# Performance work log

Measured on AMD Instinct MI355X. Metric: run time of the kernel, lower is better.

Reference implementation:

```python
import jax, jax.numpy as jnp
import numpy as np

CONTEXT = 3  # config['context']
B, H, W = 8, 256, 256
NBR = 2 * CONTEXT  # number of similarity branches


def _conv(x, w, b):
    # x: [N, Cin, H, W], w: [Cout, Cin, kh, kw], SAME padding, stride 1
    y = jax.lax.conv_general_dilated(x, w, (1, 1), 'SAME',
                                     dimension_numbers=('NCHW', 'OIHW', 'NCHW'))
    return y + b[None, :, None, None]


def setup_inputs() -> dict:
    key = jax.random.key(0)
    ks = jax.random.split(key, 5)
    x = jax.random.normal(ks[0], (B, 2 * CONTEXT + 1, H, W), dtype=jnp.float32)
    # kaiming-ish scaled inits
    W1 = jax.random.normal(ks[1], (NBR, 64, 2, 3, 3), dtype=jnp.float32) * (2.0 / (64 * 9)) ** 0.5
    b1 = jnp.zeros((NBR, 64), dtype=jnp.float32)
    W2 = jax.random.normal(ks[2], (NBR, 1, 64, 1, 1), dtype=jnp.float32) * (2.0 / 1) ** 0.5 * 0.1
    b2 = jnp.zeros((NBR, 1), dtype=jnp.float32)
    Wm = jax.random.normal(ks[3], (7, 7, 3, 3), dtype=jnp.float32) * (2.0 / (7 * 9)) ** 0.5
    bm = jnp.zeros((7,), dtype=jnp.float32)
    return {'x': x, 'W1': W1, 'b1': b1, 'W2': W2, 'b2': b2, 'Wm': Wm, 'bm': bm}


def reference(x, W1, b1, W2, b2, Wm, bm):
    # mode == 'context' path just returns x; this implements the main path.
    base = x[:, CONTEXT:CONTEXT + 1]                                  # [B,1,H,W]
    checks = jnp.concatenate([x[:, :CONTEXT], x[:, CONTEXT + 1:]], axis=1)  # [B,6,H,W]
    check_e = checks[:, :, None]                                      # [B,6,1,H,W]
    base_e = jnp.broadcast_to(base[:, None], check_e.shape)           # [B,6,1,H,W]
    # channel order: pre-frames -> (base, check); post-frames -> (check, base)
    ch0 = jnp.concatenate([base_e[:, :CONTEXT], check_e[:, CONTEXT:]], axis=2 - 2 + 2)  # placeholder
    ch0 = jnp.concatenate([base_e[:, :CONTEXT], check_e[:, CONTEXT:]], axis=1)
    ch1 = jnp.concatenate([check_e[:, :CONTEXT], base_e[:, CONTEXT:]], axis=1)
    pairs = jnp.concatenate([ch0, ch1], axis=2)                       # [B,6,2,H,W]
    pairs = jnp.swapaxes(pairs, 0, 1)                                 # [6,B,2,H,W]

    def branch(pair, w1, bb1, w2, bb2):
        h = jax.nn.relu(_conv(pair, w1, bb1))                         # [B,64,H,W]
        return jax.nn.sigmoid(_conv(h, w2, bb2))                      # [B,1,H,W]

    sims = jax.vmap(branch)(pairs, W1, b1, W2, b2)                    # [6,B,1,H,W]
    weighted = sims[:, :, 0] * jnp.swapaxes(checks, 0, 1)             # [6,B,H,W]
    weighted = jnp.swapaxes(weighted, 0, 1)                           # [B,6,H,W]
    combined = jnp.concatenate([weighted[:, :CONTEXT], base, weighted[:, CONTEXT:]], axis=1)  # [B,7,H,W]
    return _conv(combined, Wm, bm)                                    # [B,7,H,W]
```

## Files before the change

kernel.cpp:

```cpp
#include <hip/hip_runtime.h>
#include <math.h>

#define Bn 8
#define Hn 256
#define Wn 256
#define HW (Hn * Wn)
#define ROWS 8
#define RP 264
#define ZW (20 * RP)

typedef __attribute__((ext_vector_type(8))) short bf16x8;
typedef __attribute__((ext_vector_type(4))) float f32x4;

__device__ __forceinline__ unsigned int pk_bits(unsigned int lo,
                                                unsigned int hi) {
  return __builtin_amdgcn_perm(hi, lo, 0x07060302u);
}
__device__ __forceinline__ unsigned int pk_bf16(float lo, float hi) {
  return pk_bits(__float_as_uint(lo), __float_as_uint(hi));
}

__device__ __constant__ const int T0c[8] = {0, 1, 2, 9, 10, 11, 3, 4};
__device__ __constant__ const int T1c[8] = {6, 7, 8, 15, 16, 17, 12, 13};
__device__ __constant__ const int T2c[8] = {5, 14, -1, -1, -1, -1, -1, -1};

__global__ __launch_bounds__(256) void sim_kernel(
    const float* __restrict__ x,
    const float* __restrict__ W1,
    const float* __restrict__ b1,
    const float* __restrict__ W2,
    const float* __restrict__ b2,
    float* __restrict__ comb)
{
  __shared__ float rowsF[20 * RP + 64];
  __shared__ uint4 wq[4][64];

  int bi = blockIdx.x;
  int n  = bi >> 8;
  int b  = (bi >> 5) & 7;
  int h0 = (bi & 31) * ROWS;
  int cc = (n < 3) ? n : n + 1;
  int t = threadIdx.x;

  const float* xb     = x + (size_t)b * 7 * HW;
  const float* basep  = xb + 3 * HW;
  const float* checkp = xb + (size_t)cc * HW;

  {
    int f = t >> 6, qq = (t >> 4) & 3, m = t & 15;
    int bsrc = (n < 3) ? 0 : 1;
    const float* wch = W1 + ((size_t)(n * 64 + 16 * f + m)) * 18;
    unsigned int kv[4];
#pragma unroll
    for (int jj = 0; jj < 4; ++jj) {
      int ja = 2 * jj, jb = 2 * jj + 1;
      int ta = (qq == 0) ? T0c[ja] : (qq == 1) ? T1c[ja]
               : (qq == 2) ? T2c[ja] : -1;
      int tb = (qq == 0) ? T0c[jb] : (qq == 1) ? T1c[jb]
               : (qq == 2) ? T2c[jb] : -1;
      float va = 0.f, vb = 0.f;
      if (ta >= 0) {
        int pl = ta / 9, rem = ta - pl * 9;
        va = wch[(pl ? 1 - bsrc : bsrc) * 9 + rem];
      }
      if (tb >= 0) {
        int pl = tb / 9, rem = tb - pl * 9;
        vb = wch[(pl ? 1 - bsrc : bsrc) * 9 + rem];
      }
      kv[jj] = pk_bf16(va, vb);
    }
    wq[f][(qq << 4) + m] = make_uint4(kv[0], kv[1], kv[2], kv[3]);
  }

  int lane = t & 63, wvid = t >> 6;
  int q = lane >> 4, m_ = lane & 15;
  float w2v[4][4];
  f32x4 b1vv[4];
#pragma unroll
  for (int f = 0; f < 4; ++f) {
    float4 tw = *(const float4*)&W2[n * 64 + 16 * f + 4 * q];
    float4 tb = *(const float4*)&b1[n * 64 + 16 * f + 4 * q];
    w2v[f][0] = tw.x; w2v[f][1] = tw.y; w2v[f][2] = tw.z; w2v[f][3] = tw.w;
    b1vv[f][0] = tb.x; b1vv[f][1] = tb.y;
    b1vv[f][2] = tb.z; b1vv[f][3] = tb.w;
  }
  float bb = b2[n];

  {
    int col = (t & 63) << 2;
#pragma unroll
    for (int it = 0; it < 5; ++it) {
      int rf = it * 4 + (t >> 6);
      int pl = (rf >= 10) ? 1 : 0;
      int j  = rf - pl * 10;
      int hh = h0 - 1 + j;
      const float* src = pl ? checkp : basep;
      float4 val = make_float4(0.f, 0.f, 0.f, 0.f);
      if ((unsigned)hh < (unsigned)Hn)
        val = *(const float4*)(src + hh * Wn + col);
      *(float4*)&rowsF[rf * RP + 4 + col] = val;
    }
    if (t < 20) {
      rowsF[t * RP + 3] = 0.f;
      rowsF[t * RP + 260] = 0.f;
    }
    if (t >= 192) rowsF[ZW + (t - 192)] = 0.f;
  }

  const unsigned int* rowsU = (const unsigned int*)rowsF;
  unsigned int addr[8], vbit[8];
#pragma unroll
  for (int jh = 0; jh < 8; ++jh) {
    int tap = (q == 0) ? T0c[jh] : (q == 1) ? T1c[jh]
              : (q == 2) ? T2c[jh] : -1;
    if (tap >= 0) {
      int pl = tap / 9, rem = tap - pl * 9;
      int rr = rem / 3, dx = rem - rr * 3;
      addr[jh] = (pl * 10 + rr) * RP + 3 + dx + wvid * 64 + m_;
      vbit[jh] = 1u;
    } else {
      addr[jh] = (unsigned)ZW;
      vbit[jh] = 0u;
    }
  }

  __syncthreads();

  bf16x8 afrag[4];
#pragma unroll
  for (int f = 0; f < 4; ++f) afrag[f] = *(const bf16x8*)&wq[f][lane];

  float* combcc = comb + ((size_t)b * 7 + cc) * HW;
  float* comb3  = comb + ((size_t)b * 7 + 3) * HW;
  int pxs = wvid * 64 + lane;

#pragma unroll 1
  for (int r = 0; r < ROWS; ++r) {
    int h = h0 + r;
    unsigned int rowoff = (unsigned)(r * RP);

    unsigned int base[8];
#pragma unroll
    for (int jh = 0; jh < 8; ++jh) base[jh] = addr[jh] + vbit[jh] * rowoff;

    float g[4];
#pragma unroll
    for (int half = 0; half < 2; ++half) {
      unsigned int dlo[8], dhi[8];
#pragma unroll
      for (int jh = 0; jh < 8; ++jh) {
        dlo[jh] = rowsU[base[jh] + half * 32];
        dhi[jh] = rowsU[base[jh] + half * 32 + 16];
      }
#pragma unroll
      for (int j = 0; j < 2; ++j) {
        const unsigned int* d = j ? dhi : dlo;
        union { unsigned int u[4]; bf16x8 v; } bu;
#pragma unroll
        for (int jj = 0; jj < 4; ++jj)
          bu.u[jj] = pk_bits(d[2 * jj], d[2 * jj + 1]);

        f32x4 acc[4];
#pragma unroll
        for (int f = 0; f < 4; ++f)
          acc[f] = __builtin_amdgcn_mfma_f32_16x16x32_bf16(afrag[f], bu.v,
                                                           b1vv[f], 0, 0, 0);

        float sp = 0.f;
#pragma unroll
        for (int f = 0; f < 4; ++f)
#pragma unroll
          for (int rr = 0; rr < 4; ++rr)
            sp = fmaf(w2v[f][rr], fmaxf(acc[f][rr], 0.f), sp);
        sp += __shfl_xor(sp, 16, 64);
        sp += __shfl_xor(sp, 32, 64);
        sp += bb;

        float e = __builtin_amdgcn_exp2f(sp * -1.442695041f);
        g[2 * half + j] = __builtin_amdgcn_rcpf(1.f + e);
      }
    }

    int hi = lane >> 4;
    float gsel = (hi == 0) ? g[0] : (hi == 1) ? g[1] : (hi == 2) ? g[2] : g[3];
    float ccv = rowsF[(10 + r + 1) * RP + 4 + pxs];
    combcc[h * Wn + pxs] = gsel * ccv;
    if (n == 0) comb3[h * Wn + pxs] = rowsF[(r + 1) * RP + 4 + pxs];
  }
}

__global__ __launch_bounds__(256) void mix_kernel(
    const float* __restrict__ comb,
    const float* __restrict__ Wm,
    const float* __restrict__ bm,
    float* __restrict__ out)
{
  __shared__ float mr[28 * RP];

  int bi = blockIdx.x;
  int b  = bi >> 7;
  int h0 = (bi & 127) << 1;
  int t = threadIdx.x;

  for (int u = t; u < 28 * 64; u += 256) {
    int rf = u >> 6;
    int col = (u & 63) << 2;
    int ic = rf >> 2, j = rf & 3;
    int hh = h0 - 1 + j;
    float4 v = make_float4(0.f, 0.f, 0.f, 0.f);
    if ((unsigned)hh < (unsigned)Hn)
      v = *(const float4*)(comb + ((size_t)b * 7 + ic) * HW + hh * Wn + col);
    *(float4*)&mr[rf * RP + 4 + col] = v;
  }
  if (t < 28) {
    mr[t * RP + 3] = 0.f;
    mr[t * RP + 260] = 0.f;
  }
  __syncthreads();

  int r   = t >> 7;
  int px0 = (t & 127) << 1;
  int h   = h0 + r;

  float acc[7][2];
#pragma unroll
  for (int oc = 0; oc < 7; ++oc) {
    float bv = bm[oc];
    acc[oc][0] = bv;
    acc[oc][1] = bv;
  }

#pragma unroll 1
  for (int ic = 0; ic < 7; ++ic) {
    float w[3][4];
#pragma unroll
    for (int dy = 0; dy < 3; ++dy) {
      const float* rp = &mr[(ic * 4 + r + dy) * RP + 3 + px0];
      w[dy][0] = rp[0]; w[dy][1] = rp[1];
      w[dy][2] = rp[2]; w[dy][3] = rp[3];
    }
    const float* wp = Wm + ic * 9;
#pragma unroll
    for (int oc = 0; oc < 7; ++oc) {
      const float* wo = wp + oc * 63;
#pragma unroll
      for (int dy = 0; dy < 3; ++dy)
#pragma unroll
        for (int dx = 0; dx < 3; ++dx) {
          float wvv = wo[dy * 3 + dx];
          acc[oc][0] = fmaf(wvv, w[dy][0 + dx], acc[oc][0]);
          acc[oc][1] = fmaf(wvv, w[dy][1 + dx], acc[oc][1]);
        }
    }
  }

  float* ob = out + (size_t)b * 7 * HW + h * Wn + px0;
#pragma unroll
  for (int oc = 0; oc < 7; ++oc)
    *(float2*)(ob + (size_t)oc * HW) = make_float2(acc[oc][0], acc[oc][1]);
}

extern "C" void kernel_launch(void* const* d_in, const int* in_sizes, int n_in,
                              void* d_out, int out_size, void* d_ws, size_t ws_size,
                              hipStream_t stream) {
  const float* x  = (const float*)d_in[0];
  const float* W1 = (const float*)d_in[1];
  const float* b1 = (const float*)d_in[2];
  const float* W2 = (const float*)d_in[3];
  const float* b2 = (const float*)d_in[4];
  const float* Wm = (const float*)d_in[5];
  const float* bm = (const float*)d_in[6];
  float* out  = (float*)d_out;
  float* comb = (float*)d_ws;

  sim_kernel<<<6 * 8 * (Hn / ROWS), 256, 0, stream>>>(x, W1, b1, W2, b2, comb);
  mix_kernel<<<8 * (Hn / 2), 256, 0, stream>>>(comb, Wm, bm, out);
}
```

Before: 120.7 us.

## Read base channel from input in mix kernel, enlarge mix tiles, pack epilogue FMAs

The sim kernel no longer copies the base frame into the workspace. The mix kernel reads that channel directly from x, which removes one write and read of a full plane. The mix kernel now handles 4 rows per block with 512 threads, so the halo overhead per output row is smaller, at the cost of more shared memory per block. The sim kernel also swaps per-row address recomputation for incremental address steps, and packs the ReLU/W2 dot product into 2-wide vector operations that could map to packed FMA instructions.

```diff
diff --git a/kernel.cpp b/kernel.cpp
--- a/kernel.cpp
+++ b/kernel.cpp
@@ -11,6 +11,7 @@
 
 typedef __attribute__((ext_vector_type(8))) short bf16x8;
 typedef __attribute__((ext_vector_type(4))) float f32x4;
+typedef __attribute__((ext_vector_type(2))) float f32x2;
 
 __device__ __forceinline__ unsigned int pk_bits(unsigned int lo,
                                                 unsigned int hi) {
@@ -74,13 +75,14 @@
 
   int lane = t & 63, wvid = t >> 6;
   int q = lane >> 4, m_ = lane & 15;
-  float w2v[4][4];
+  f32x2 w2A[4], w2B[4];
   f32x4 b1vv[4];
 #pragma unroll
   for (int f = 0; f < 4; ++f) {
     float4 tw = *(const float4*)&W2[n * 64 + 16 * f + 4 * q];
     float4 tb = *(const float4*)&b1[n * 64 + 16 * f + 4 * q];
-    w2v[f][0] = tw.x; w2v[f][1] = tw.y; w2v[f][2] = tw.z; w2v[f][3] = tw.w;
+    w2A[f][0] = tw.x; w2A[f][1] = tw.y;
+    w2B[f][0] = tw.z; w2B[f][1] = tw.w;
     b1vv[f][0] = tb.x; b1vv[f][1] = tb.y;
     b1vv[f][2] = tb.z; b1vv[f][3] = tb.w;
   }
@@ -108,7 +110,7 @@
   }
 
   const unsigned int* rowsU = (const unsigned int*)rowsF;
-  unsigned int addr[8], vbit[8];
+  unsigned int addr[8], step[8];
 #pragma unroll
   for (int jh = 0; jh < 8; ++jh) {
     int tap = (q == 0) ? T0c[jh] : (q == 1) ? T1c[jh]
@@ -117,10 +119,10 @@
       int pl = tap / 9, rem = tap - pl * 9;
       int rr = rem / 3, dx = rem - rr * 3;
       addr[jh] = (pl * 10 + rr) * RP + 3 + dx + wvid * 64 + m_;
-      vbit[jh] = 1u;
+      step[jh] = (unsigned)RP;
     } else {
       addr[jh] = (unsigned)ZW;
-      vbit[jh] = 0u;
+      step[jh] = 0u;
     }
   }
 
@@ -131,17 +133,11 @@
   for (int f = 0; f < 4; ++f) afrag[f] = *(const bf16x8*)&wq[f][lane];
 
   float* combcc = comb + ((size_t)b * 7 + cc) * HW;
-  float* comb3  = comb + ((size_t)b * 7 + 3) * HW;
   int pxs = wvid * 64 + lane;
 
 #pragma unroll 1
   for (int r = 0; r < ROWS; ++r) {
     int h = h0 + r;
-    unsigned int rowoff = (unsigned)(r * RP);
-
-    unsigned int base[8];
-#pragma unroll
-    for (int jh = 0; jh < 8; ++jh) base[jh] = addr[jh] + vbit[jh] * rowoff;
 
     float g[4];
 #pragma unroll
@@ -149,8 +145,8 @@
       unsigned int dlo[8], dhi[8];
 #pragma unroll
       for (int jh = 0; jh < 8; ++jh) {
-        dlo[jh] = rowsU[base[jh] + half * 32];
-        dhi[jh] = rowsU[base[jh] + half * 32 + 16];
+        dlo[jh] = rowsU[addr[jh] + half * 32];
+        dhi[jh] = rowsU[addr[jh] + half * 32 + 16];
       }
 #pragma unroll
       for (int j = 0; j < 2; ++j) {
@@ -166,12 +162,18 @@
           acc[f] = __builtin_amdgcn_mfma_f32_16x16x32_bf16(afrag[f], bu.v,
                                                            b1vv[f], 0, 0, 0);
 
-        float sp = 0.f;
-#pragma unroll
-        for (int f = 0; f < 4; ++f)
-#pragma unroll
-          for (int rr = 0; rr < 4; ++rr)
-            sp = fmaf(w2v[f][rr], fmaxf(acc[f][rr], 0.f), sp);
+        f32x2 sA = {0.f, 0.f}, sB = {0.f, 0.f};
+#pragma unroll
+        for (int f = 0; f < 4; ++f) {
+          f32x2 a01, a23;
+          a01[0] = acc[f][0]; a01[1] = acc[f][1];
+          a23[0] = acc[f][2]; a23[1] = acc[f][3];
+          a01 = __builtin_elementwise_max(a01, (f32x2)0.f);
+          a23 = __builtin_elementwise_max(a23, (f32x2)0.f);
+          sA += w2A[f] * a01;
+          sB += w2B[f] * a23;
+        }
+        float sp = (sA[0] + sB[0]) + (sA[1] + sB[1]);
         sp += __shfl_xor(sp, 16, 64);
         sp += __shfl_xor(sp, 32, 64);
         sp += bb;
@@ -185,34 +187,39 @@
     float gsel = (hi == 0) ? g[0] : (hi == 1) ? g[1] : (hi == 2) ? g[2] : g[3];
     float ccv = rowsF[(10 + r + 1) * RP + 4 + pxs];
     combcc[h * Wn + pxs] = gsel * ccv;
-    if (n == 0) comb3[h * Wn + pxs] = rowsF[(r + 1) * RP + 4 + pxs];
-  }
-}
-
-__global__ __launch_bounds__(256) void mix_kernel(
+
+#pragma unroll
+    for (int jh = 0; jh < 8; ++jh) addr[jh] += step[jh];
+  }
+}
+
+__global__ __launch_bounds__(512) void mix_kernel(
     const float* __restrict__ comb,
+    const float* __restrict__ x,
     const float* __restrict__ Wm,
     const float* __restrict__ bm,
     float* __restrict__ out)
 {
-  __shared__ float mr[28 * RP];
+  __shared__ float mr[42 * RP];
 
   int bi = blockIdx.x;
-  int b  = bi >> 7;
-  int h0 = (bi & 127) << 1;
+  int b  = bi >> 6;
+  int h0 = (bi & 63) << 2;
   int t = threadIdx.x;
 
-  for (int u = t; u < 28 * 64; u += 256) {
+  for (int u = t; u < 42 * 64; u += 512) {
     int rf = u >> 6;
     int col = (u & 63) << 2;
-    int ic = rf >> 2, j = rf & 3;
+    int ic = rf / 6, j = rf - ic * 6;
     int hh = h0 - 1 + j;
+    const float* src = (ic == 3) ? (x + ((size_t)b * 7 + 3) * HW)
+                                 : (comb + ((size_t)b * 7 + ic) * HW);
     float4 v = make_float4(0.f, 0.f, 0.f, 0.f);
     if ((unsigned)hh < (unsigned)Hn)
-      v = *(const float4*)(comb + ((size_t)b * 7 + ic) * HW + hh * Wn + col);
+      v = *(const float4*)(src + hh * Wn + col);
     *(float4*)&mr[rf * RP + 4 + col] = v;
   }
-  if (t < 28) {
+  if (t < 42) {
     mr[t * RP + 3] = 0.f;
     mr[t * RP + 260] = 0.f;
   }
@@ -235,7 +242,7 @@
     float w[3][4];
 #pragma unroll
     for (int dy = 0; dy < 3; ++dy) {
-      const float* rp = &mr[(ic * 4 + r + dy) * RP + 3 + px0];
+      const float* rp = &mr[(ic * 6 + r + dy) * RP + 3 + px0];
       w[dy][0] = rp[0]; w[dy][1] = rp[1];
       w[dy][2] = rp[2]; w[dy][3] = rp[3];
     }
@@ -274,5 +281,5 @@
   float* comb = (float*)d_ws;
 
   sim_kernel<<<6 * 8 * (Hn / ROWS), 256, 0, stream>>>(x, W1, b1, W2, b2, comb);
-  mix_kernel<<<8 * (Hn / 2), 256, 0, stream>>>(comb, Wm, bm, out);
-}
+  mix_kernel<<<8 * (Hn / 4), 512, 0, stream>>>(comb, x, Wm, bm, out);
+}
```

Result: faster. 118.2 us (-2.0%).
